# Kernel tuning notes

Hardware: AMD Instinct MI355X
Metric: run time of the kernel (lower is better)

## Reference

```python
import jax, jax.numpy as jnp
import numpy as np
from jax import lax

N, T, D_IN = 8192, 64, 64
R = 256            # reservoir_dim
K = 3              # diffusion hops
D_OUT = 64
E = 131072
LEAK = 0.3
SPECTRAL_RADIUS = 0.9
SPARSITY = 0.9


def setup_inputs() -> dict:
    key = jax.random.key(0)
    kx, ke = jax.random.split(key)
    rng = np.random.default_rng(0)

    # ESN fixed buffers (match torch init: randn*0.1; sparse randn scaled to rho)
    W_in = (rng.standard_normal((R, D_IN)) * 0.1).astype(np.float32)
    W_res = rng.standard_normal((R, R)).astype(np.float32)
    mask = rng.random((R, R)) < SPARSITY
    W_res[mask] = 0.0
    rho = float(np.abs(np.linalg.eigvals(W_res)).max())
    if rho > 1e-8:
        W_res = W_res * (SPECTRAL_RADIUS / rho)

    # readout: Linear((K+1)*R -> 2*D_OUT), GELU, Linear(2*D_OUT -> D_OUT), LayerNorm
    fan1 = (K + 1) * R
    W1 = (rng.standard_normal((2 * D_OUT, fan1)) / np.sqrt(fan1)).astype(np.float32)
    b1 = np.zeros((2 * D_OUT,), np.float32)
    W2 = (rng.standard_normal((D_OUT, 2 * D_OUT)) / np.sqrt(2 * D_OUT)).astype(np.float32)
    b2 = np.zeros((D_OUT,), np.float32)
    gamma = np.ones((D_OUT,), np.float32)
    beta = np.zeros((D_OUT,), np.float32)

    x = jax.random.normal(kx, (N, T, D_IN), dtype=jnp.float32)
    edge_index = jax.random.randint(ke, (2, E), 0, N, dtype=jnp.int64)

    return {
        "x": x,
        "edge_index": edge_index,
        "W_in": jnp.asarray(W_in),
        "W_res": jnp.asarray(W_res),
        "W1": jnp.asarray(W1), "b1": jnp.asarray(b1),
        "W2": jnp.asarray(W2), "b2": jnp.asarray(b2),
        "gamma": jnp.asarray(gamma), "beta": jnp.asarray(beta),
    }


def _esn(x, W_in, W_res):
    # x: [N, T, D_IN] -> final reservoir state [N, R]
    x_proj = jnp.einsum("ntd,rd->tnr", x, W_in)  # [T, N, R]

    def step(h, xp_t):
        h_new = jnp.tanh(xp_t + h @ W_res.T)
        return (1.0 - LEAK) * h + LEAK * h_new, None

    h0 = jnp.zeros((x.shape[0], W_res.shape[0]), dtype=x.dtype)
    h, _ = lax.scan(step, h0, x_proj)
    return h


def _norm_adj(edge_index, n_nodes):
    # symmetric D^{-1/2} A D^{-1/2}; dedup handled by idempotent .set
    row = jnp.concatenate([edge_index[0], edge_index[1]])
    col = jnp.concatenate([edge_index[1], edge_index[0]])
    A_bin = jnp.zeros((n_nodes, n_nodes), jnp.float32).at[row, col].set(1.0)
    deg = A_bin.sum(axis=1)
    dinv = jnp.where(deg > 0, 1.0 / jnp.sqrt(jnp.maximum(deg, 1e-12)), 0.0)
    dinv = jnp.minimum(dinv, 1e6)
    return dinv[:, None] * A_bin * dinv[None, :]


def reference(x, edge_index, W_in, W_res, W1, b1, W2, b2, gamma, beta):
    h = _esn(x, W_in, W_res)                    # [N, R]
    A = _norm_adj(edge_index, x.shape[0])       # [N, N]

    diffused = [h]
    h_k = h
    for _ in range(K):
        h_k = A @ h_k
        diffused.append(h_k)
    cat = jnp.concatenate(diffused, axis=-1)    # [N, (K+1)*R]

    z = jax.nn.gelu(cat @ W1.T + b1, approximate=False)
    z = z @ W2.T + b2                           # [N, D_OUT]
    mu = z.mean(axis=-1, keepdims=True)
    var = z.var(axis=-1, keepdims=True)
    z = (z - mu) / jnp.sqrt(var + 1e-5)
    return z * gamma + beta
```

## Files before the change

kernel.cpp:

```cpp
#include <hip/hip_runtime.h>
#include <hip/hip_bf16.h>
#include <hip/hip_fp16.h>
#include <math.h>

#define NN    8192
#define TT    64
#define DIN   64
#define RR    256
#define DOUT  64
#define HID   128
#define CATD  1024
#define NE    131072
#define MASKW 256
#define MAXD  256
#define HROW  328
#define C8ROW 768

typedef __attribute__((ext_vector_type(8))) short    s16x8;
typedef __attribute__((ext_vector_type(8))) _Float16 f16x8;
typedef __attribute__((ext_vector_type(4))) float    f32x4;
typedef __attribute__((ext_vector_type(2))) float    f32x2;

static __device__ __forceinline__ unsigned short f2bs(float f) {
  union { __hip_bfloat16 b; unsigned short u; } cv;
  cv.b = __float2bfloat16(f);
  return cv.u;
}
static __device__ __forceinline__ unsigned int pack2bf(float a, float b) {
  return (unsigned int)f2bs(a) | ((unsigned int)f2bs(b) << 16);
}
static __device__ __forceinline__ unsigned int pack2h(float a, float b) {
  return (unsigned int)__half_as_ushort(__float2half(a))
       | ((unsigned int)__half_as_ushort(__float2half(b)) << 16);
}
static __device__ __forceinline__ unsigned int pack4fp8(float a, float b, float c, float d) {
  unsigned int p = 0;
  p = __builtin_amdgcn_cvt_pk_fp8_f32(a, b, (int)p, false);
  p = __builtin_amdgcn_cvt_pk_fp8_f32(c, d, (int)p, true);
  return p;
}


__global__ __launch_bounds__(256) void setup_kernel(
    uint4* __restrict__ mask4,
    const float* __restrict__ Wres, const float* __restrict__ Win,
    const float* __restrict__ W1, const float* __restrict__ W2,
    unsigned short* __restrict__ wresh, unsigned short* __restrict__ winh,
    unsigned short* __restrict__ W1h, unsigned short* __restrict__ W2h) {
  int i = blockIdx.x * 256 + threadIdx.x;
  mask4[i] = make_uint4(0u, 0u, 0u, 0u);
  if (i < 65536) wresh[i] = f2bs(Wres[i]);
  else if (i < 81920) winh[i - 65536] = f2bs(Win[i - 65536]);
  else if (i < 212992) W1h[i - 81920] = __half_as_ushort(__float2half(W1[i - 81920]));
  else if (i < 221184) W2h[i - 212992] = __half_as_ushort(__float2half(W2[i - 212992]));
}

__global__ __launch_bounds__(256) void edge_kernel(const int* __restrict__ eidx,
                                                   unsigned int* __restrict__ mask) {
  int e = blockIdx.x * 256 + threadIdx.x;
  if (e < NE) {
    int u = eidx[e];
    int v = eidx[NE + e];
    atomicOr(&mask[(size_t)u * MASKW + (v >> 5)], 1u << (v & 31));
    atomicOr(&mask[(size_t)v * MASKW + (u >> 5)], 1u << (u & 31));
  }
}

__global__ __launch_bounds__(256) void nbrlist_kernel(const unsigned int* __restrict__ mask,
                                                      unsigned short* __restrict__ nbrlist,
                                                      int* __restrict__ nbrcnt,
                                                      float* __restrict__ dinv) {
  __shared__ int wsum[4];
  const int n = blockIdx.x;
  const int tid = threadIdx.x;
  const int lane = tid & 63;
  const int w = tid >> 6;
  unsigned int m = mask[(size_t)n * MASKW + tid];
  const int c = __popc(m);
  int inc = c;
#pragma unroll
  for (int d = 1; d < 64; d <<= 1) {
    int v = __shfl_up(inc, d, 64);
    if (lane >= d) inc += v;
  }
  if (lane == 63) wsum[w] = inc;
  __syncthreads();
  int base = 0;
  for (int i = 0; i < w; ++i) base += wsum[i];
  int off = base + inc - c;
  while (m) {
    int b = __ffs(m) - 1;
    m &= m - 1;
    if (off < MAXD) nbrlist[(size_t)n * MAXD + off] = (unsigned short)(tid * 32 + b);
    ++off;
  }
  if (tid == 255) {
    int tot = base + inc;
    nbrcnt[n] = tot < MAXD ? tot : MAXD;
    dinv[n] = (tot > 0) ? fminf(rsqrtf((float)tot), 1e6f) : 0.0f;
  }
}

__global__ __launch_bounds__(512, 4) void esn_mfma_kernel(
    const float* __restrict__ x,
    const unsigned short* __restrict__ winh,
    const unsigned short* __restrict__ wresh,
    unsigned short* __restrict__ cat,
    unsigned char* __restrict__ cat8)
{
  __shared__ unsigned short hs[2][16][HROW];
  const int tid  = threadIdx.x;
  const int lane = tid & 63;
  const int w    = tid >> 6;
  const int lr   = lane & 15;
  const int lg   = lane >> 4;
  const int sn   = tid >> 5;
  const int sq   = tid & 31;
  const long gn0 = (long)blockIdx.x * 16;
  const int bx   = (lr >> 3) & 1;
  const int lgx  = lg ^ bx;
  const int lgw  = (lg >> 1) ^ bx;
  const int bs   = (sn >> 3) & 1;

  s16x8 waug[2][10];
#pragma unroll
  for (int rt = 0; rt < 2; ++rt) {
    const int r = w * 32 + rt * 16 + lr;
#pragma unroll
    for (int kt = 0; kt < 8; ++kt)
      waug[rt][kt] = *(const s16x8*)(wresh + r * RR + kt * 32 + lg * 8);
#pragma unroll
    for (int kt = 8; kt < 10; ++kt)
      waug[rt][kt] = *(const s16x8*)(winh + r * DIN + (kt - 8) * 32 + lg * 8);
  }

  unsigned short* const rd0 = &hs[0][0][0] + lr * HROW + lgx * 8;
  unsigned short* const rd1 = &hs[1][0][0] + lr * HROW + lgx * 8;
  unsigned short* const wh0 = &hs[0][0][0] + lr * HROW + (w * 4 + lgw) * 8 + (lg & 1) * 4;
  unsigned short* const wh1 = &hs[1][0][0] + lr * HROW + (w * 4 + lgw) * 8 + (lg & 1) * 4;
  unsigned short* const xs0 = &hs[0][0][0] + sn * HROW + (32 + ((sq >> 2) ^ bs)) * 8 + (sq & 3) * 2;
  unsigned short* const xs1 = &hs[1][0][0] + sn * HROW + (32 + ((sq >> 2) ^ bs)) * 8 + (sq & 3) * 2;

  for (int i = tid; i < 16 * HROW / 2; i += 512) ((unsigned int*)hs[0])[i] = 0u;

  const float* xrow = x + (gn0 + sn) * (long)(TT * DIN) + sq * 2;
  float2 xr0 = *(const float2*)(xrow);
  float2 xr1 = *(const float2*)(xrow + DIN);
  __syncthreads();
  *(unsigned int*)xs0 = pack2bf(xr0.x, xr0.y);
  xr0 = *(const float2*)(xrow + 2 * DIN);

  f32x4 hreg[2];
  hreg[0] = (f32x4){0.f, 0.f, 0.f, 0.f};
  hreg[1] = (f32x4){0.f, 0.f, 0.f, 0.f};
  __syncthreads();

#define ESN_STEP(RD, WH, XS, XRS, XRL, TNEXT)                                        \
  {                                                                                  \
    f32x4 a0 = (f32x4){0.f,0.f,0.f,0.f}, a1 = a0;                                    \
    __builtin_amdgcn_s_setprio(1);                                                   \
    _Pragma("unroll")                                                                \
    for (int kt = 0; kt < 10; ++kt) {                                                \
      const s16x8 hb = *(const s16x8*)(RD + kt * 32);                                \
      a0 = __builtin_amdgcn_mfma_f32_16x16x32_bf16(waug[0][kt], hb, a0, 0, 0, 0);    \
      a1 = __builtin_amdgcn_mfma_f32_16x16x32_bf16(waug[1][kt], hb, a1, 0, 0, 0);    \
    }                                                                                \
    __builtin_amdgcn_s_setprio(0);                                                   \
    *(unsigned int*)(XS) = pack2bf(XRS.x, XRS.y);                 \
    XRL = *(const float2*)(xrow + (TNEXT) * DIN);                      \
    _Pragma("unroll")                                                                \
    for (int rt = 0; rt < 2; ++rt) {                                                 \
      const f32x4 ae = rt ? a1 : a0;                                                 \
      f32x4 hn;                                                                      \
      _Pragma("unroll")                                                              \
      for (int i = 0; i < 4; ++i) {                                                  \
        const float e = __builtin_amdgcn_exp2f(ae[i] * 2.8853900817779268f);         \
        const float rc = __builtin_amdgcn_rcpf(e + 1.0f);                            \
        hn[i] = fmaf(-0.6f, rc, fmaf(0.7f, hreg[rt][i], 0.3f));                      \
      }                                                                              \
      hreg[rt] = hn;                                                                 \
      *(uint2*)(WH + rt * 16) =                                                      \
          make_uint2(pack2bf(hn[0], hn[1]), pack2bf(hn[2], hn[3]));                  \
    }                                                                                \
  }

  for (int tc = 0; tc < TT / 2; ++tc) {
    const int t = tc * 2;
    const int tla = (t + 3 < TT) ? t + 3 : TT - 1;
    ESN_STEP(rd0, wh1, xs1, xr1, xr1, tla);
    __syncthreads();
    const int tlb = (t + 4 < TT) ? t + 4 : TT - 1;
    ESN_STEP(rd1, wh0, xs0, xr0, xr0, tlb);
    __syncthreads();
  }
#undef ESN_STEP

#pragma unroll
  for (int rt = 0; rt < 2; ++rt) {
    *(uint2*)(cat + (gn0 + lr) * CATD + w * 32 + rt * 16 + lg * 4) =
        make_uint2(pack2h(hreg[rt][0], hreg[rt][1]), pack2h(hreg[rt][2], hreg[rt][3]));
    *(unsigned int*)(cat8 + (gn0 + lr) * C8ROW + w * 32 + rt * 16 + lg * 4) =
        pack4fp8(hreg[rt][0], hreg[rt][1], hreg[rt][2], hreg[rt][3]);
  }
}

__global__ __launch_bounds__(256) void spmv_kernel(
    const unsigned short* __restrict__ nbrlist, const int* __restrict__ nbrcnt,
    const float* __restrict__ dinv, unsigned short* __restrict__ cat,
    unsigned char* __restrict__ cat8, int hop)
{
  const int wv   = threadIdx.x >> 6;
  const int lane = threadIdx.x & 63;
  const int half = lane >> 5;
  const int li   = lane & 31;
  const int n    = blockIdx.x * 8 + wv * 2 + half;
  const int cnt  = nbrcnt[n];
  const unsigned char* in8 = cat8 + (size_t)(hop - 1) * RR;
  float acc[8];
#pragma unroll
  for (int k = 0; k < 8; ++k) acc[k] = 0.0f;

  for (int c0 = 0; c0 < cnt; c0 += 32) {
    const int m = (cnt - c0 < 32) ? cnt - c0 : 32;
    int idx = 0; float dv = 0.f;
    if (li < m) {
      idx = (int)nbrlist[(size_t)n * MAXD + c0 + li];
      dv  = dinv[idx];
    }
#pragma unroll 8
    for (int i = 0; i < m; ++i) {
      const int   j  = __shfl(idx, half * 32 + i, 64);
      const float wj = __shfl(dv,  half * 32 + i, 64);
      const uint2 u  = *(const uint2*)(in8 + (size_t)j * C8ROW + li * 8);
      const f32x2 f0 = __builtin_amdgcn_cvt_pk_f32_fp8((int)u.x, false);
      const f32x2 f1 = __builtin_amdgcn_cvt_pk_f32_fp8((int)u.x, true);
      const f32x2 f2 = __builtin_amdgcn_cvt_pk_f32_fp8((int)u.y, false);
      const f32x2 f3 = __builtin_amdgcn_cvt_pk_f32_fp8((int)u.y, true);
      acc[0] += wj * f0[0]; acc[1] += wj * f0[1];
      acc[2] += wj * f1[0]; acc[3] += wj * f1[1];
      acc[4] += wj * f2[0]; acc[5] += wj * f2[1];
      acc[6] += wj * f3[0]; acc[7] += wj * f3[1];
    }
  }
  const float dn = dinv[n];
#pragma unroll
  for (int k = 0; k < 8; ++k) acc[k] *= dn;
  uint4 o;
  o.x = pack2h(acc[0], acc[1]);
  o.y = pack2h(acc[2], acc[3]);
  o.z = pack2h(acc[4], acc[5]);
  o.w = pack2h(acc[6], acc[7]);
  *(uint4*)(cat + (size_t)n * CATD + (size_t)hop * RR + li * 8) = o;
  if (hop < 3) {
    uint2 o8;
    o8.x = pack4fp8(acc[0], acc[1], acc[2], acc[3]);
    o8.y = pack4fp8(acc[4], acc[5], acc[6], acc[7]);
    *(uint2*)(cat8 + (size_t)n * C8ROW + (size_t)hop * RR + li * 8) = o8;
  }
}

__global__ __launch_bounds__(256) void readout_kernel(
    const unsigned short* __restrict__ cat,
    const unsigned short* __restrict__ W1h,
    const float* __restrict__ b1,
    const unsigned short* __restrict__ W2h,
    const float* __restrict__ b2, const float* __restrict__ gamma,
    const float* __restrict__ beta, float* __restrict__ out)
{
  __shared__ unsigned short z1[32][136];
  __shared__ float z2[32][68];
  const int tid  = threadIdx.x;
  const int lane = tid & 63;
  const int w    = tid >> 6;
  const int lr   = lane & 15;
  const int lg   = lane >> 4;
  const long gn0 = (long)blockIdx.x * 32;

  f32x4 a00 = (f32x4){0.f,0.f,0.f,0.f}, a01 = a00, a10 = a00, a11 = a00;
  const unsigned short* arow0 = cat + (gn0 + lr) * CATD;
  const unsigned short* arow1 = cat + (gn0 + 16 + lr) * CATD;
  const unsigned short* brow0 = W1h + (w * 32 + lr) * CATD;
  const unsigned short* brow1 = W1h + (w * 32 + 16 + lr) * CATD;
#pragma unroll 8
  for (int kt = 0; kt < 32; ++kt) {
    const f16x8 af0 = *(const f16x8*)(arow0 + kt * 32 + lg * 8);
    const f16x8 af1 = *(const f16x8*)(arow1 + kt * 32 + lg * 8);
    const f16x8 bf0 = *(const f16x8*)(brow0 + kt * 32 + lg * 8);
    const f16x8 bf1 = *(const f16x8*)(brow1 + kt * 32 + lg * 8);
    a00 = __builtin_amdgcn_mfma_f32_16x16x32_f16(af0, bf0, a00, 0, 0, 0);
    a01 = __builtin_amdgcn_mfma_f32_16x16x32_f16(af0, bf1, a01, 0, 0, 0);
    a10 = __builtin_amdgcn_mfma_f32_16x16x32_f16(af1, bf0, a10, 0, 0, 0);
    a11 = __builtin_amdgcn_mfma_f32_16x16x32_f16(af1, bf1, a11, 0, 0, 0);
  }
  const float is2 = 0.70710678118654752f;
#pragma unroll
  for (int nt = 0; nt < 2; ++nt) {
#pragma unroll
    for (int ht = 0; ht < 2; ++ht) {
      const int hid = w * 32 + ht * 16 + lr;
      const float bb = b1[hid];
      const f32x4 a = nt ? (ht ? a11 : a10) : (ht ? a01 : a00);
#pragma unroll
      for (int i = 0; i < 4; ++i) {
        const float v = a[i] + bb;
        const float g = 0.5f * v * (1.0f + erff(v * is2));
        z1[nt * 16 + lg * 4 + i][hid] = __half_as_ushort(__float2half(g));
      }
    }
  }
  __syncthreads();

  f32x4 c20 = (f32x4){0.f,0.f,0.f,0.f}, c21 = c20;
  const unsigned short* w2row = W2h + (w * 16 + lr) * HID;
#pragma unroll
  for (int kt = 0; kt < 4; ++kt) {
    const f16x8 bf  = *(const f16x8*)(w2row + kt * 32 + lg * 8);
    const f16x8 af0 = *(const f16x8*)(&z1[lr][kt * 32 + lg * 8]);
    const f16x8 af1 = *(const f16x8*)(&z1[16 + lr][kt * 32 + lg * 8]);
    c20 = __builtin_amdgcn_mfma_f32_16x16x32_f16(af0, bf, c20, 0, 0, 0);
    c21 = __builtin_amdgcn_mfma_f32_16x16x32_f16(af1, bf, c21, 0, 0, 0);
  }
  {
    const float bb = b2[w * 16 + lr];
#pragma unroll
    for (int i = 0; i < 4; ++i) {
      z2[lg * 4 + i][w * 16 + lr]      = c20[i] + bb;
      z2[16 + lg * 4 + i][w * 16 + lr] = c21[i] + bb;
    }
  }
  __syncthreads();

  {
    const int n = tid >> 3;
    const int c = tid & 7;
    float v[8], s = 0.0f, s2 = 0.0f;
#pragma unroll
    for (int k2 = 0; k2 < 8; ++k2) {
      v[k2] = z2[n][c + 8 * k2];
      s += v[k2]; s2 += v[k2] * v[k2];
    }
#pragma unroll
    for (int m = 1; m < 8; m <<= 1) {
      s  += __shfl_xor(s,  m, 64);
      s2 += __shfl_xor(s2, m, 64);
    }
    const float mu  = s * (1.0f / 64.0f);
    const float var = s2 * (1.0f / 64.0f) - mu * mu;
    const float inv = rsqrtf(var + 1e-5f);
    float* orow = out + (gn0 + n) * DOUT;
#pragma unroll
    for (int k2 = 0; k2 < 8; ++k2)
      orow[c + 8 * k2] = (v[k2] - mu) * inv * gamma[c + 8 * k2] + beta[c + 8 * k2];
  }
}


extern "C" void kernel_launch(void* const* d_in, const int* in_sizes, int n_in,
                              void* d_out, int out_size, void* d_ws, size_t ws_size,
                              hipStream_t stream) {
  const float* x     = (const float*)d_in[0];
  const int*   eidx  = (const int*)d_in[1];
  const float* W_in  = (const float*)d_in[2];
  const float* W_res = (const float*)d_in[3];
  const float* W1    = (const float*)d_in[4];
  const float* b1    = (const float*)d_in[5];
  const float* W2    = (const float*)d_in[6];
  const float* b2    = (const float*)d_in[7];
  const float* gamma = (const float*)d_in[8];
  const float* beta  = (const float*)d_in[9];
  float* out = (float*)d_out;

  char* ws = (char*)d_ws;
  size_t off = 0;
  auto alloc = [&](size_t bytes) {
    void* p = ws + off;
    off += (bytes + 255) & ~(size_t)255;
    return p;
  };
  unsigned int*   mask    = (unsigned int*)  alloc((size_t)NN * MASKW * 4);
  unsigned short* cat     = (unsigned short*)alloc((size_t)NN * CATD * 2);
  unsigned char*  cat8    = (unsigned char*) alloc((size_t)NN * C8ROW);
  unsigned short* nbrlist = (unsigned short*)alloc((size_t)NN * MAXD * 2);
  int*            nbrcnt  = (int*)           alloc((size_t)NN * 4);
  float*          dinv    = (float*)         alloc((size_t)NN * 4);
  unsigned short* wresh   = (unsigned short*)alloc((size_t)RR * RR * 2);
  unsigned short* winh    = (unsigned short*)alloc((size_t)RR * DIN * 2);
  unsigned short* W1h     = (unsigned short*)alloc((size_t)HID * CATD * 2);
  unsigned short* W2h     = (unsigned short*)alloc((size_t)DOUT * HID * 2);

  setup_kernel<<<2048, 256, 0, stream>>>((uint4*)mask, W_res, W_in, W1, W2,
                                         wresh, winh, W1h, W2h);
  edge_kernel<<<NE / 256, 256, 0, stream>>>(eidx, mask);
  nbrlist_kernel<<<NN, 256, 0, stream>>>(mask, nbrlist, nbrcnt, dinv);

  esn_mfma_kernel<<<NN / 16, 512, 0, stream>>>(x, winh, wresh, cat, cat8);

  for (int k = 1; k <= 3; ++k)
    spmv_kernel<<<NN / 8, 256, 0, stream>>>(nbrlist, nbrcnt, dinv, cat, cat8, k);

  readout_kernel<<<NN / 32, 256, 0, stream>>>(cat, W1h, b1, W2h, b2, gamma, beta, out);
}
```

Measured before the change: 183.7 us.

## Feed ESN input fragments to MFMA from registers and prefetch SpMV neighbor chunks

The ESN kernel no longer stages bf16-converted x tiles through shared memory. Each lane loads its own x fragment straight from global memory into registers in MFMA operand layout, two timesteps ahead, and the LDS row shrinks to match. This removes LDS writes and reads for the input projection but adds scattered global loads on the recurrent critical path. Separately, the SpMV kernel prefetches the next chunk of neighbor indices and degree scalings while the current chunk is processed, which hides some gather latency when a node has many neighbors.

New measurement: 373.6 us. 2.03x slower.

```diff
diff --git a/kernel.cpp b/kernel.cpp
--- a/kernel.cpp
+++ b/kernel.cpp
@@ -13,7 +13,7 @@
 #define NE    131072
 #define MASKW 256
 #define MAXD  256
-#define HROW  328
+#define HROW  264
 #define C8ROW 768
 
 typedef __attribute__((ext_vector_type(8))) short    s16x8;
@@ -38,6 +38,14 @@
   p = __builtin_amdgcn_cvt_pk_fp8_f32(a, b, (int)p, false);
   p = __builtin_amdgcn_cvt_pk_fp8_f32(c, d, (int)p, true);
   return p;
+}
+static __device__ __forceinline__ s16x8 load_xfrag(const float* p) {
+  const float4 f0 = *(const float4*)(p);
+  const float4 f1 = *(const float4*)(p + 4);
+  union { uint4 u; s16x8 v; } cv;
+  cv.u = make_uint4(pack2bf(f0.x, f0.y), pack2bf(f0.z, f0.w),
+                    pack2bf(f1.x, f1.y), pack2bf(f1.z, f1.w));
+  return cv.v;
 }
 
 
@@ -114,13 +122,10 @@
   const int w    = tid >> 6;
   const int lr   = lane & 15;
   const int lg   = lane >> 4;
-  const int sn   = tid >> 5;
-  const int sq   = tid & 31;
   const long gn0 = (long)blockIdx.x * 16;
   const int bx   = (lr >> 3) & 1;
   const int lgx  = lg ^ bx;
   const int lgw  = (lg >> 1) ^ bx;
-  const int bs   = (sn >> 3) & 1;
 
   s16x8 waug[2][10];
 #pragma unroll
@@ -138,36 +143,38 @@
   unsigned short* const rd1 = &hs[1][0][0] + lr * HROW + lgx * 8;
   unsigned short* const wh0 = &hs[0][0][0] + lr * HROW + (w * 4 + lgw) * 8 + (lg & 1) * 4;
   unsigned short* const wh1 = &hs[1][0][0] + lr * HROW + (w * 4 + lgw) * 8 + (lg & 1) * 4;
-  unsigned short* const xs0 = &hs[0][0][0] + sn * HROW + (32 + ((sq >> 2) ^ bs)) * 8 + (sq & 3) * 2;
-  unsigned short* const xs1 = &hs[1][0][0] + sn * HROW + (32 + ((sq >> 2) ^ bs)) * 8 + (sq & 3) * 2;
 
   for (int i = tid; i < 16 * HROW / 2; i += 512) ((unsigned int*)hs[0])[i] = 0u;
 
-  const float* xrow = x + (gn0 + sn) * (long)(TT * DIN) + sq * 2;
-  float2 xr0 = *(const float2*)(xrow);
-  float2 xr1 = *(const float2*)(xrow + DIN);
-  __syncthreads();
-  *(unsigned int*)xs0 = pack2bf(xr0.x, xr0.y);
-  xr0 = *(const float2*)(xrow + 2 * DIN);
+  const float* xw = x + (gn0 + lr) * (long)(TT * DIN) + lg * 8;
+  s16x8 xa0 = load_xfrag(xw);
+  s16x8 xa1 = load_xfrag(xw + 32);
+  s16x8 xb0 = load_xfrag(xw + DIN);
+  s16x8 xb1 = load_xfrag(xw + DIN + 32);
 
   f32x4 hreg[2];
   hreg[0] = (f32x4){0.f, 0.f, 0.f, 0.f};
   hreg[1] = (f32x4){0.f, 0.f, 0.f, 0.f};
   __syncthreads();
 
-#define ESN_STEP(RD, WH, XS, XRS, XRL, TNEXT)                                        \
+#define ESN_STEP(RD, WH, X0, X1, TN)                                                 \
   {                                                                                  \
     f32x4 a0 = (f32x4){0.f,0.f,0.f,0.f}, a1 = a0;                                    \
     __builtin_amdgcn_s_setprio(1);                                                   \
     _Pragma("unroll")                                                                \
-    for (int kt = 0; kt < 10; ++kt) {                                                \
+    for (int kt = 0; kt < 8; ++kt) {                                                 \
       const s16x8 hb = *(const s16x8*)(RD + kt * 32);                                \
       a0 = __builtin_amdgcn_mfma_f32_16x16x32_bf16(waug[0][kt], hb, a0, 0, 0, 0);    \
       a1 = __builtin_amdgcn_mfma_f32_16x16x32_bf16(waug[1][kt], hb, a1, 0, 0, 0);    \
     }                                                                                \
+    a0 = __builtin_amdgcn_mfma_f32_16x16x32_bf16(waug[0][8], X0, a0, 0, 0, 0);       \
+    a1 = __builtin_amdgcn_mfma_f32_16x16x32_bf16(waug[1][8], X0, a1, 0, 0, 0);       \
+    a0 = __builtin_amdgcn_mfma_f32_16x16x32_bf16(waug[0][9], X1, a0, 0, 0, 0);       \
+    a1 = __builtin_amdgcn_mfma_f32_16x16x32_bf16(waug[1][9], X1, a1, 0, 0, 0);       \
     __builtin_amdgcn_s_setprio(0);                                                   \
-    *(unsigned int*)(XS) = pack2bf(XRS.x, XRS.y);                 \
-    XRL = *(const float2*)(xrow + (TNEXT) * DIN);                      \
+                \
+    X0 = load_xfrag(xw + (TN) * DIN);                                                \
+    X1 = load_xfrag(xw + (TN) * DIN + 32);                                           \
     _Pragma("unroll")                                                                \
     for (int rt = 0; rt < 2; ++rt) {                                                 \
       const f32x4 ae = rt ? a1 : a0;                                                 \
@@ -186,11 +193,11 @@
 
   for (int tc = 0; tc < TT / 2; ++tc) {
     const int t = tc * 2;
-    const int tla = (t + 3 < TT) ? t + 3 : TT - 1;
-    ESN_STEP(rd0, wh1, xs1, xr1, xr1, tla);
+    const int tla = (t + 2 < TT) ? t + 2 : TT - 1;
+    ESN_STEP(rd0, wh1, xa0, xa1, tla);
     __syncthreads();
-    const int tlb = (t + 4 < TT) ? t + 4 : TT - 1;
-    ESN_STEP(rd1, wh0, xs0, xr0, xr0, tlb);
+    const int tlb = (t + 3 < TT) ? t + 3 : TT - 1;
+    ESN_STEP(rd1, wh0, xb0, xb1, tlb);
     __syncthreads();
   }
 #undef ESN_STEP
@@ -220,12 +227,17 @@
 #pragma unroll
   for (int k = 0; k < 8; ++k) acc[k] = 0.0f;
 
+  int idx = 0; float dv = 0.f;
+  if (li < cnt) {
+    idx = (int)nbrlist[(size_t)n * MAXD + li];
+    dv  = dinv[idx];
+  }
   for (int c0 = 0; c0 < cnt; c0 += 32) {
     const int m = (cnt - c0 < 32) ? cnt - c0 : 32;
-    int idx = 0; float dv = 0.f;
-    if (li < m) {
-      idx = (int)nbrlist[(size_t)n * MAXD + c0 + li];
-      dv  = dinv[idx];
+    int idxn = 0; float dvn = 0.f;
+    if (c0 + 32 + li < cnt) {
+      idxn = (int)nbrlist[(size_t)n * MAXD + c0 + 32 + li];
+      dvn  = dinv[idxn];
     }
 #pragma unroll 8
     for (int i = 0; i < m; ++i) {
@@ -241,6 +253,7 @@
       acc[4] += wj * f2[0]; acc[5] += wj * f2[1];
       acc[6] += wj * f3[0]; acc[7] += wj * f3[1];
     }
+    idx = idxn; dv = dvn;
   }
   const float dn = dinv[n];
 #pragma unroll
```
